# Kernel optimization log

Measured on AMD Instinct MI355X. Metric: run time of the kernel, lower is better.

The kernel has to match this reference:

```python
import jax, jax.numpy as jnp
import numpy as np

BN_EPS = 1e-5

def _vq(x, embed):
    # x: (..., dim), embed: (dim, K). Nearest-codeword lookup with straight-through.
    dim = x.shape[-1]
    flat = x.reshape(-1, dim)
    dist = (flat * flat).sum(1, keepdims=True) - 2.0 * (flat @ embed) + (embed * embed).sum(0, keepdims=True)
    ids = jnp.argmin(dist, axis=1)
    q = jnp.take(embed.T, ids, axis=0).reshape(x.shape)
    diff = jnp.mean((jax.lax.stop_gradient(q) - x) ** 2)
    q = x + jax.lax.stop_gradient(q - x)
    return q, diff

def _weight_quantize(W, embed, in_mem, out_mem):
    # W: (out_f, in_f). Group W.T into (out_g, in_g, in_mem*out_mem) blocks,
    # VQ each block, scatter back to (out_f, in_f). Matches torch chunk/stack loops.
    out_f, in_f = W.shape
    in_g, out_g = in_f // in_mem, out_f // out_mem
    g = W.T.reshape(in_g, in_mem, out_g, out_mem).transpose(2, 0, 1, 3).reshape(out_g, in_g, in_mem * out_mem)
    q, diff = _vq(g, embed)
    qW = q.reshape(out_g, in_g, in_mem, out_mem).transpose(0, 3, 1, 2).reshape(out_f, in_f)
    return qW, diff

def _bn(x, gamma, beta):
    # training-mode BatchNorm1d: biased batch variance
    mu = x.mean(axis=0)
    var = ((x - mu) ** 2).mean(axis=0)
    return (x - mu) * jax.lax.rsqrt(var + BN_EPS) * gamma + beta


def setup_inputs() -> dict:
    key = jax.random.key(0)
    ks = jax.random.split(key, 8)
    B, D_IN, H, D_OUT, K = 65536, 784, 512, 10, 512
    s = 0.05
    return {
        "x": jax.random.normal(ks[0], (B, D_IN), jnp.float32),
        "W1": jax.random.normal(ks[1], (H, D_IN), jnp.float32) * s,
        "b1": jnp.zeros((H,), jnp.float32),
        "gamma1": jnp.ones((H,), jnp.float32),
        "beta1": jnp.zeros((H,), jnp.float32),
        "E1": jax.random.normal(ks[2], (28, K), jnp.float32) * s,  # dim = in_mem(7)*out_mem(4)
        "W2": jax.random.normal(ks[3], (H, H), jnp.float32) * s,
        "b2": jnp.zeros((H,), jnp.float32),
        "E2": jax.random.normal(ks[4], (16, K), jnp.float32) * s,  # dim = in_mem(16)*out_mem(1)
        "W3": jax.random.normal(ks[5], (D_OUT, H), jnp.float32) * s,
        "b3": jnp.zeros((D_OUT,), jnp.float32),
    }


def reference(x, W1, b1, gamma1, beta1, E1, W2, b2, E2, W3, b3):
    qW1, diff1 = _weight_quantize(W1, E1, 7, 4)
    h = jax.nn.relu(x @ qW1.T + b1)
    qW2, diff2 = _weight_quantize(W2, E2, 16, 1)
    h = jax.nn.relu(_bn(h, gamma1, beta1) @ qW2.T + b2)
    out = h @ W3.T + b3
    return out, diff1 + diff2
```

## Files before the change

### kernel.cpp

```cpp
#include <hip/hip_runtime.h>
#include <stdint.h>

#define BATCH   65536
#define D_IN    784
#define KP      800
#define HDIM    512
#define D_OUT   10
#define NCODE   512
#define HT_LD   520

typedef _Float16 f16;
typedef _Float16 f16x8 __attribute__((ext_vector_type(8)));
typedef float    f32x4 __attribute__((ext_vector_type(4)));

__device__ __forceinline__ void gld_lds16(const void* g, void* l) {
  __builtin_amdgcn_global_load_lds((const __attribute__((address_space(1))) void*)g,
                                   (__attribute__((address_space(3))) void*)l, 16, 0, 0);
}

#define MEMFENCE asm volatile("" ::: "memory")
#define BARRIER() do { MEMFENCE; __builtin_amdgcn_s_barrier(); MEMFENCE; } while (0)

__global__ void k_vq1(const float* __restrict__ W1, const float* __restrict__ E1,
                      f16* __restrict__ qW1, float* __restrict__ diffacc) {
  #pragma clang fp contract(off)
  __shared__ float E1s[28 * NCODE];
  __shared__ float Ts[NCODE];
  for (int i = threadIdx.x; i < 28 * NCODE; i += 256) E1s[i] = E1[i];
  __syncthreads();
  for (int k = threadIdx.x; k < NCODE; k += 256) {
    float e0 = E1s[k];
    float t = e0 * e0;
    for (int j = 1; j < 28; ++j) {
      float e = E1s[j * NCODE + k];
      float ee = e * e;
      t = t + ee;
    }
    Ts[k] = t;
  }
  __syncthreads();
  const int wid = threadIdx.x >> 6, lane = threadIdx.x & 63;
  const int bid = blockIdx.x * 4 + wid;
  const int og = bid / 112, ig = bid % 112;
  float v[28], vv[28];
  #pragma unroll
  for (int j = 0; j < 28; ++j) {
    int om = j & 3, im = j >> 2;
    v[j] = W1[(og * 4 + om) * D_IN + ig * 7 + im];
    vv[j] = v[j] * v[j];
  }
  float r[8];
  #pragma unroll
  for (int j = 0; j < 8; ++j) r[j] = vv[j];
  #pragma unroll
  for (int j = 0; j < 8; ++j) r[j] = r[j] + vv[8 + j];
  #pragma unroll
  for (int j = 0; j < 8; ++j) r[j] = r[j] + vv[16 + j];
  float s = ((r[0] + r[1]) + (r[2] + r[3])) + ((r[4] + r[5]) + (r[6] + r[7]));
  s = s + vv[24]; s = s + vv[25]; s = s + vv[26]; s = s + vv[27];

  float bestd = 1e30f; int bestk = 0x7fffffff;
  for (int t = 0; t < 8; ++t) {
    int k = t * 64 + lane;
    float dot = 0.f;
    #pragma unroll
    for (int j = 0; j < 28; ++j) dot = __builtin_fmaf(v[j], E1s[j * NCODE + k], dot);
    float d = (s - 2.0f * dot) + Ts[k];
    if (d < bestd || (d == bestd && k < bestk)) { bestd = d; bestk = k; }
  }
  for (int off = 32; off; off >>= 1) {
    float d2 = __shfl_down(bestd, off, 64);
    int   k2 = __shfl_down(bestk, off, 64);
    if (d2 < bestd || (d2 == bestd && k2 < bestk)) { bestd = d2; bestk = k2; }
  }
  int kstar = __shfl(bestk, 0, 64);
  float sq = 0.f;
  if (lane < 28) {
    int om = lane & 3, im = lane >> 2;
    float q = E1s[lane * NCODE + kstar];
    qW1[(size_t)(og * 4 + om) * KP + ig * 7 + im] = (f16)q;
    float dd = q - v[lane]; sq = dd * dd;
  }
  for (int off = 32; off; off >>= 1) sq += __shfl_down(sq, off, 64);
  if (lane == 0) atomicAdd(&diffacc[bid & 127], sq);
}

__global__ void k_vq2(const float* __restrict__ W2, const float* __restrict__ E2,
                      f16* __restrict__ qW2, float* __restrict__ diffacc) {
  #pragma clang fp contract(off)
  __shared__ float E2s[16 * NCODE];
  __shared__ float Ts[NCODE];
  for (int i = threadIdx.x; i < 16 * NCODE; i += 256) E2s[i] = E2[i];
  __syncthreads();
  for (int k = threadIdx.x; k < NCODE; k += 256) {
    float e0 = E2s[k];
    float t = e0 * e0;
    for (int j = 1; j < 16; ++j) {
      float e = E2s[j * NCODE + k];
      float ee = e * e;
      t = t + ee;
    }
    Ts[k] = t;
  }
  __syncthreads();
  const int wid = threadIdx.x >> 6, lane = threadIdx.x & 63;
  const int bid = blockIdx.x * 4 + wid;
  const int og = bid >> 5, ig = bid & 31;
  float v[16], vv[16];
  #pragma unroll
  for (int j = 0; j < 16; ++j) {
    v[j] = W2[og * HDIM + ig * 16 + j];
    vv[j] = v[j] * v[j];
  }
  float r[8];
  #pragma unroll
  for (int j = 0; j < 8; ++j) r[j] = vv[j];
  #pragma unroll
  for (int j = 0; j < 8; ++j) r[j] = r[j] + vv[8 + j];
  float s = ((r[0] + r[1]) + (r[2] + r[3])) + ((r[4] + r[5]) + (r[6] + r[7]));

  float bestd = 1e30f; int bestk = 0x7fffffff;
  for (int t = 0; t < 8; ++t) {
    int k = t * 64 + lane;
    float dot = 0.f;
    #pragma unroll
    for (int j = 0; j < 16; ++j) dot = __builtin_fmaf(v[j], E2s[j * NCODE + k], dot);
    float d = (s - 2.0f * dot) + Ts[k];
    if (d < bestd || (d == bestd && k < bestk)) { bestd = d; bestk = k; }
  }
  for (int off = 32; off; off >>= 1) {
    float d2 = __shfl_down(bestd, off, 64);
    int   k2 = __shfl_down(bestk, off, 64);
    if (d2 < bestd || (d2 == bestd && k2 < bestk)) { bestd = d2; bestk = k2; }
  }
  int kstar = __shfl(bestk, 0, 64);
  float sq = 0.f;
  if (lane < 16) {
    float q = E2s[lane * NCODE + kstar];
    qW2[(size_t)og * HDIM + ig * 16 + lane] = (f16)q;
    float dd = q - v[lane]; sq = dd * dd;
  }
  for (int off = 32; off; off >>= 1) sq += __shfl_down(sq, off, 64);
  if (lane == 0) atomicAdd(&diffacc[bid & 127], sq);
}

__global__ void __launch_bounds__(512, 2)
k_gemm1(const float* __restrict__ X, const f16* __restrict__ Bw,
        const float* __restrict__ bias, f16* __restrict__ C,
        float* __restrict__ statacc) {
  __shared__ __align__(16) char lds_all[HT_LD * 128 * 2];
  __shared__ float cls[512], cls2[512];
  f16* ht = (f16*)lds_all;
  const int tid = threadIdx.x;
  const int bm = blockIdx.x;
  const int lane = tid & 63, wid = tid >> 6;
  const int waveM = wid & 1, waveN = wid >> 1;
  const int l15 = lane & 15, quad = lane >> 4;

  cls[tid] = 0.f; cls2[tid] = 0.f;

  const int rA = tid >> 2, cA = tid & 3;
  const float* gArow = X + (size_t)(bm * 128 + rA) * D_IN;
  const int wAoff = rA * 32 + ((cA ^ ((rA >> 1) & 3)) * 8);
  const f16* gBp[4]; int lBoff[4];
  #pragma unroll
  for (int i = 0; i < 4; ++i) {
    int s = tid + i * 512;
    int rB = s >> 2, cB = s & 3;
    gBp[i] = Bw + (size_t)rB * KP + ((cB ^ ((rB >> 1) & 3)) * 8);
    lBoff[i] = s * 8;
  }

  f32x4 acc[4][8];
  #pragma unroll
  for (int i = 0; i < 4; ++i)
    #pragma unroll
    for (int j = 0; j < 8; ++j) acc[i][j] = (f32x4){0.f, 0.f, 0.f, 0.f};

  const int cs_l = (l15 >> 1) & 3;
  const int aoff = (waveM * 64 + l15) * 32;
  const int boff = (waveN * 128 + l15) * 32;
  const int qoff = (quad ^ cs_l) * 8;

  float4 ra0, ra1;
  auto issueA = [&](int k0) {
    int gc = k0 + cA * 8;
    int gco = gc < D_IN ? gc : 0;
    ra0 = *(const float4*)(gArow + gco);
    ra1 = *(const float4*)(gArow + gco + 4);
  };
  auto writeA = [&](int k0, char* buf) {
    float4 a0 = ra0, a1 = ra1;
    if (k0 + cA * 8 >= D_IN) { a0 = (float4){0.f,0.f,0.f,0.f}; a1 = a0; }
    f16x8 o;
    o[0]=(f16)a0.x; o[1]=(f16)a0.y; o[2]=(f16)a0.z; o[3]=(f16)a0.w;
    o[4]=(f16)a1.x; o[5]=(f16)a1.y; o[6]=(f16)a1.z; o[7]=(f16)a1.w;
    *(f16x8*)((f16*)buf + wAoff) = o;
  };
  auto issueB = [&](int k0, char* buf) {
    f16* Bs_ = (f16*)(buf + 8192);
    #pragma unroll
    for (int i = 0; i < 4; ++i) gld_lds16(gBp[i] + k0, Bs_ + lBoff[i]);
  };
  auto mma = [&](const char* buf) {
    const f16* As_ = (const f16*)buf;
    const f16* Bs_ = (const f16*)(buf + 8192);
    f16x8 af[4], bf[8];
    #pragma unroll
    for (int i = 0; i < 4; ++i) af[i] = *(const f16x8*)(As_ + aoff + i * 512 + qoff);
    #pragma unroll
    for (int j = 0; j < 8; ++j) bf[j] = *(const f16x8*)(Bs_ + boff + j * 512 + qoff);
    #pragma unroll
    for (int i = 0; i < 4; ++i)
      #pragma unroll
      for (int j = 0; j < 8; ++j)
        acc[i][j] = __builtin_amdgcn_mfma_f32_16x16x32_f16(af[i], bf[j], acc[i][j], 0, 0, 0);
  };

  const int NT = KP / 32;

  issueA(0);  MEMFENCE;
  issueB(0, lds_all);          MEMFENCE;
  issueB(32, lds_all + 40960); MEMFENCE;
  writeA(0, lds_all);
  MEMFENCE;
  issueA(32); MEMFENCE;
  asm volatile("s_waitcnt vmcnt(6) lgkmcnt(0)" ::: "memory");
  BARRIER();

  int cur = 0;
  for (int k = 0; k < NT; ++k) {
    int n1 = cur + 40960; if (n1 == 122880) n1 = 0;
    int n2 = n1 + 40960;  if (n2 == 122880) n2 = 0;
    if (k + 2 < NT) { issueB((k + 2) * 32, lds_all + n2); }
    MEMFENCE;
    __builtin_amdgcn_s_setprio(1);
    mma(lds_all + cur);
    __builtin_amdgcn_s_setprio(0);
    if (k + 1 < NT) {
      MEMFENCE;
      writeA((k + 1) * 32, lds_all + n1);
      MEMFENCE;
      if (k + 2 < NT) {
        issueA((k + 2) * 32); MEMFENCE;
        asm volatile("s_waitcnt vmcnt(6) lgkmcnt(0)" ::: "memory");
      } else {
        asm volatile("s_waitcnt vmcnt(0) lgkmcnt(0)" ::: "memory");
      }
    }
    BARRIER();
    cur = n1;
  }

  const int colbase = waveN * 128 + l15;
  float bcol[8];
  #pragma unroll
  for (int j = 0; j < 8; ++j) bcol[j] = bias[colbase + j * 16];
  float cs[8], cs2[8];
  #pragma unroll
  for (int j = 0; j < 8; ++j) { cs[j] = 0.f; cs2[j] = 0.f; }
  #pragma unroll
  for (int i = 0; i < 4; ++i)
    #pragma unroll
    for (int r2 = 0; r2 < 4; ++r2) {
      int rloc = waveM * 64 + i * 16 + quad * 4 + r2;
      #pragma unroll
      for (int j = 0; j < 8; ++j) {
        float v = acc[i][j][r2] + bcol[j];
        v = v > 0.f ? v : 0.f;
        ht[rloc * HT_LD + waveN * 128 + j * 16 + l15] = (f16)v;
        cs[j] += v; cs2[j] += v * v;
      }
    }
  #pragma unroll
  for (int j = 0; j < 8; ++j) {
    cs[j]  += __shfl_xor(cs[j], 16, 64);  cs[j]  += __shfl_xor(cs[j], 32, 64);
    cs2[j] += __shfl_xor(cs2[j], 16, 64); cs2[j] += __shfl_xor(cs2[j], 32, 64);
  }
  if (quad == 0) {
    #pragma unroll
    for (int j = 0; j < 8; ++j) {
      atomicAdd(&cls[waveN * 128 + j * 16 + l15], cs[j]);
      atomicAdd(&cls2[waveN * 128 + j * 16 + l15], cs2[j]);
    }
  }
  __syncthreads();
  atomicAdd(&statacc[256 + tid], cls[tid]);
  atomicAdd(&statacc[768 + tid], cls2[tid]);
  #pragma unroll
  for (int rr = 0; rr < 16; ++rr) {
    int row = wid * 16 + rr;
    f16x8 vrow = *(const f16x8*)(ht + row * HT_LD + lane * 8);
    *(f16x8*)(C + (size_t)(bm * 128 + row) * HDIM + lane * 8) = vrow;
  }
}

__global__ void k_bnprep(const float* __restrict__ acc, const float* __restrict__ gamma,
                         const float* __restrict__ beta, float* __restrict__ ab,
                         const float* __restrict__ W3, f16* __restrict__ W3h,
                         float* __restrict__ diff_out) {
  const int c = threadIdx.x;
  const float inv = 1.f / 65536.f;
  float mu = acc[256 + c] * inv;
  float msq = acc[768 + c] * inv;
  float var = msq - mu * mu;
  float a = gamma[c] / sqrtf(var + 1e-5f);
  ab[c] = a;
  ab[512 + c] = beta[c] - mu * a;
  #pragma unroll
  for (int o = 0; o < 16; ++o)
    W3h[o * HDIM + c] = (o < D_OUT) ? (f16)W3[o * HDIM + c] : (f16)0.f;
  if (c == 0) {
    float s1 = 0.f, s2 = 0.f;
    for (int i = 0; i < 128; ++i) { s1 += acc[i]; s2 += acc[128 + i]; }
    diff_out[0] = s1 * (1.f / 401408.f) + s2 * (1.f / 262144.f);
  }
}

__global__ void k_bnfold(f16* __restrict__ qW2, const float* __restrict__ ab,
                         const float* __restrict__ b2, float* __restrict__ bias2) {
  __shared__ float red[256];
  const int n = blockIdx.x, t = threadIdx.x;
  float partial = 0.f;
  #pragma unroll
  for (int kk = 0; kk < 2; ++kk) {
    int k = t + kk * 256;
    float w = (float)qW2[n * HDIM + k];
    partial += ab[512 + k] * w;
    qW2[n * HDIM + k] = (f16)(ab[k] * w);
  }
  red[t] = partial; __syncthreads();
  for (int s = 128; s > 0; s >>= 1) { if (t < s) red[t] += red[t + s]; __syncthreads(); }
  if (t == 0) bias2[n] = b2[n] + red[0];
}

__global__ void __launch_bounds__(512, 2)
k_gemm2f(const f16* __restrict__ A, const f16* __restrict__ Bw,
         const float* __restrict__ bias2, const f16* __restrict__ W3h,
         const float* __restrict__ b3, float* __restrict__ out) {
  __shared__ __align__(16) char lds_all[HT_LD * 128 * 2];
  f16* ht = (f16*)lds_all;
  const int tid = threadIdx.x;
  const int bm = blockIdx.x;
  const int lane = tid & 63, wid = tid >> 6;
  const int waveM = wid & 1, waveN = wid >> 1;
  const int l15 = lane & 15, quad = lane >> 4;

  const int rA = tid >> 2, cA = tid & 3;
  const f16* gAp = A + (size_t)(bm * 128 + rA) * HDIM + ((cA ^ ((rA >> 1) & 3)) * 8);
  const int lAoff = tid * 8;
  const f16* gBp[4]; int lBoff[4];
  #pragma unroll
  for (int i = 0; i < 4; ++i) {
    int s = tid + i * 512;
    int rB = s >> 2, cB = s & 3;
    gBp[i] = Bw + (size_t)rB * HDIM + ((cB ^ ((rB >> 1) & 3)) * 8);
    lBoff[i] = s * 8;
  }

  f32x4 acc[4][8];
  #pragma unroll
  for (int i = 0; i < 4; ++i)
    #pragma unroll
    for (int j = 0; j < 8; ++j) acc[i][j] = (f32x4){0.f, 0.f, 0.f, 0.f};

  const int cs_l = (l15 >> 1) & 3;
  const int aoff = (waveM * 64 + l15) * 32;
  const int boff = (waveN * 128 + l15) * 32;
  const int qoff = (quad ^ cs_l) * 8;

  auto issueT = [&](int k0, char* buf) {
    f16* As_ = (f16*)buf;
    f16* Bs_ = (f16*)(buf + 8192);
    gld_lds16(gAp + k0, As_ + lAoff);
    #pragma unroll
    for (int i = 0; i < 4; ++i) gld_lds16(gBp[i] + k0, Bs_ + lBoff[i]);
  };
  auto mma = [&](const char* buf) {
    const f16* As_ = (const f16*)buf;
    const f16* Bs_ = (const f16*)(buf + 8192);
    f16x8 af[4], bf[8];
    #pragma unroll
    for (int i = 0; i < 4; ++i) af[i] = *(const f16x8*)(As_ + aoff + i * 512 + qoff);
    #pragma unroll
    for (int j = 0; j < 8; ++j) bf[j] = *(const f16x8*)(Bs_ + boff + j * 512 + qoff);
    #pragma unroll
    for (int i = 0; i < 4; ++i)
      #pragma unroll
      for (int j = 0; j < 8; ++j)
        acc[i][j] = __builtin_amdgcn_mfma_f32_16x16x32_f16(af[i], bf[j], acc[i][j], 0, 0, 0);
  };

  const int NT = HDIM / 32;

  issueT(0, lds_all);          MEMFENCE;
  issueT(32, lds_all + 40960); MEMFENCE;
  asm volatile("s_waitcnt vmcnt(5)" ::: "memory");
  BARRIER();

  int cur = 0;
  for (int k = 0; k < NT; ++k) {
    int n1 = cur + 40960; if (n1 == 122880) n1 = 0;
    int n2 = n1 + 40960;  if (n2 == 122880) n2 = 0;
    if (k + 2 < NT) { issueT((k + 2) * 32, lds_all + n2); }
    MEMFENCE;
    __builtin_amdgcn_s_setprio(1);
    mma(lds_all + cur);
    __builtin_amdgcn_s_setprio(0);
    if (k + 2 < NT)      asm volatile("s_waitcnt vmcnt(5)" ::: "memory");
    else if (k + 1 < NT) asm volatile("s_waitcnt vmcnt(0)" ::: "memory");
    BARRIER();
    cur = n1;
  }

  const int colbase = waveN * 128 + l15;
  float bcol[8];
  #pragma unroll
  for (int j = 0; j < 8; ++j) bcol[j] = bias2[colbase + j * 16];
  #pragma unroll
  for (int i = 0; i < 4; ++i)
    #pragma unroll
    for (int r2 = 0; r2 < 4; ++r2) {
      int rloc = waveM * 64 + i * 16 + quad * 4 + r2;
      #pragma unroll
      for (int j = 0; j < 8; ++j) {
        float v = acc[i][j][r2] + bcol[j];
        v = v > 0.f ? v : 0.f;
        ht[rloc * HT_LD + waveN * 128 + j * 16 + l15] = (f16)v;
      }
    }
  __syncthreads();
  f32x4 oacc = (f32x4){0.f, 0.f, 0.f, 0.f};
  #pragma unroll
  for (int ks = 0; ks < 16; ++ks) {
    f16x8 bfr = *(const f16x8*)(W3h + l15 * HDIM + ks * 32 + quad * 8);
    f16x8 afr = *(const f16x8*)(ht + (wid * 16 + l15) * HT_LD + ks * 32 + quad * 8);
    oacc = __builtin_amdgcn_mfma_f32_16x16x32_f16(afr, bfr, oacc, 0, 0, 0);
  }
  if (l15 < D_OUT) {
    float badd = b3[l15];
    #pragma unroll
    for (int r2 = 0; r2 < 4; ++r2) {
      int row = bm * 128 + wid * 16 + quad * 4 + r2;
      out[(size_t)row * D_OUT + l15] = oacc[r2] + badd;
    }
  }
}

extern "C" void kernel_launch(void* const* d_in, const int* in_sizes, int n_in,
                              void* d_out, int out_size, void* d_ws, size_t ws_size,
                              hipStream_t stream) {
  const float* x     = (const float*)d_in[0];
  const float* W1    = (const float*)d_in[1];
  const float* b1    = (const float*)d_in[2];
  const float* gamma = (const float*)d_in[3];
  const float* beta  = (const float*)d_in[4];
  const float* E1    = (const float*)d_in[5];
  const float* W2    = (const float*)d_in[6];
  const float* b2    = (const float*)d_in[7];
  const float* E2    = (const float*)d_in[8];
  const float* W3    = (const float*)d_in[9];
  const float* b3    = (const float*)d_in[10];
  float* out = (float*)d_out;

  char* ws = (char*)d_ws;
  float* accum = (float*)ws;
  f16* qW1h = (f16*)(ws + 8192);
  f16* qW2h = (f16*)(ws + 827392);
  f16* W3h  = (f16*)(ws + 1351680);
  float* ab = (float*)(ws + 1368064);
  float* bias2 = (float*)(ws + 1372160);
  f16* h    = (f16*)(ws + 1376256);

  (void)hipMemsetAsync(ws, 0, 827392, stream);
  k_vq1<<<3584, 256, 0, stream>>>(W1, E1, qW1h, accum);
  k_vq2<<<4096, 256, 0, stream>>>(W2, E2, qW2h, accum + 128);
  k_gemm1<<<512, 512, 0, stream>>>(x, qW1h, b1, h, accum);
  k_bnprep<<<1, 512, 0, stream>>>(accum, gamma, beta, ab, W3, W3h, out + (size_t)BATCH * D_OUT);
  k_bnfold<<<512, 256, 0, stream>>>(qW2h, ab, b2, bias2);
  k_gemm2f<<<512, 512, 0, stream>>>(h, qW2h, bias2, W3h, b3, out);
}
```

Baseline: 516.6 us.

## Switch GEMM mainloops to BK=64 with single A buffer and double-buffered B

```diff
diff --git a/kernel.cpp b/kernel.cpp
--- a/kernel.cpp
+++ b/kernel.cpp
@@ -3,7 +3,7 @@
 
 #define BATCH   65536
 #define D_IN    784
-#define KP      800
+#define KP      832
 #define HDIM    512
 #define D_OUT   10
 #define NCODE   512
@@ -148,7 +148,7 @@
 k_gemm1(const float* __restrict__ X, const f16* __restrict__ Bw,
         const float* __restrict__ bias, f16* __restrict__ C,
         float* __restrict__ statacc) {
-  __shared__ __align__(16) char lds_all[HT_LD * 128 * 2];
+  __shared__ __align__(16) char lds_all[147456];
   __shared__ float cls[512], cls2[512];
   f16* ht = (f16*)lds_all;
   const int tid = threadIdx.x;
@@ -161,13 +161,14 @@
 
   const int rA = tid >> 2, cA = tid & 3;
   const float* gArow = X + (size_t)(bm * 128 + rA) * D_IN;
-  const int wAoff = rA * 32 + ((cA ^ ((rA >> 1) & 3)) * 8);
-  const f16* gBp[4]; int lBoff[4];
-  #pragma unroll
-  for (int i = 0; i < 4; ++i) {
+  const int wA0 = rA * 64 + ((cA ^ (rA & 7)) * 8);
+  const int wA1 = rA * 64 + (((cA + 4) ^ (rA & 7)) * 8);
+  const f16* gBp[8]; int lBoff[8];
+  #pragma unroll
+  for (int i = 0; i < 8; ++i) {
     int s = tid + i * 512;
-    int rB = s >> 2, cB = s & 3;
-    gBp[i] = Bw + (size_t)rB * KP + ((cB ^ ((rB >> 1) & 3)) * 8);
+    int rB = s >> 3, cB = s & 7;
+    gBp[i] = Bw + (size_t)rB * KP + ((cB ^ (rB & 7)) * 8);
     lBoff[i] = s * 8;
   }
 
@@ -177,80 +178,78 @@
     #pragma unroll
     for (int j = 0; j < 8; ++j) acc[i][j] = (f32x4){0.f, 0.f, 0.f, 0.f};
 
-  const int cs_l = (l15 >> 1) & 3;
-  const int aoff = (waveM * 64 + l15) * 32;
-  const int boff = (waveN * 128 + l15) * 32;
-  const int qoff = (quad ^ cs_l) * 8;
-
-  float4 ra0, ra1;
+  const int swz = (l15 & 7);
+  const int arow = waveM * 64 + l15;
+  const int brow = waveN * 128 + l15;
+
+  float4 ra0, ra1, ra2, ra3;
   auto issueA = [&](int k0) {
-    int gc = k0 + cA * 8;
-    int gco = gc < D_IN ? gc : 0;
-    ra0 = *(const float4*)(gArow + gco);
-    ra1 = *(const float4*)(gArow + gco + 4);
-  };
-  auto writeA = [&](int k0, char* buf) {
-    float4 a0 = ra0, a1 = ra1;
-    if (k0 + cA * 8 >= D_IN) { a0 = (float4){0.f,0.f,0.f,0.f}; a1 = a0; }
-    f16x8 o;
-    o[0]=(f16)a0.x; o[1]=(f16)a0.y; o[2]=(f16)a0.z; o[3]=(f16)a0.w;
-    o[4]=(f16)a1.x; o[5]=(f16)a1.y; o[6]=(f16)a1.z; o[7]=(f16)a1.w;
-    *(f16x8*)((f16*)buf + wAoff) = o;
-  };
-  auto issueB = [&](int k0, char* buf) {
-    f16* Bs_ = (f16*)(buf + 8192);
-    #pragma unroll
-    for (int i = 0; i < 4; ++i) gld_lds16(gBp[i] + k0, Bs_ + lBoff[i]);
-  };
-  auto mma = [&](const char* buf) {
-    const f16* As_ = (const f16*)buf;
-    const f16* Bs_ = (const f16*)(buf + 8192);
-    f16x8 af[4], bf[8];
-    #pragma unroll
-    for (int i = 0; i < 4; ++i) af[i] = *(const f16x8*)(As_ + aoff + i * 512 + qoff);
-    #pragma unroll
-    for (int j = 0; j < 8; ++j) bf[j] = *(const f16x8*)(Bs_ + boff + j * 512 + qoff);
-    #pragma unroll
-    for (int i = 0; i < 4; ++i)
-      #pragma unroll
-      for (int j = 0; j < 8; ++j)
-        acc[i][j] = __builtin_amdgcn_mfma_f32_16x16x32_f16(af[i], bf[j], acc[i][j], 0, 0, 0);
-  };
-
-  const int NT = KP / 32;
-
+    int g0 = k0 + cA * 8;
+    int g1 = k0 + (cA + 4) * 8;
+    int g0c = g0 < D_IN ? g0 : 0;
+    int g1c = g1 < D_IN ? g1 : 0;
+    ra0 = *(const float4*)(gArow + g0c);
+    ra1 = *(const float4*)(gArow + g0c + 4);
+    ra2 = *(const float4*)(gArow + g1c);
+    ra3 = *(const float4*)(gArow + g1c + 4);
+  };
+  auto writeA = [&](int k0) {
+    float4 a0 = ra0, a1 = ra1, b0 = ra2, b1 = ra3;
+    if (k0 + cA * 8 >= D_IN)       { a0 = (float4){0.f,0.f,0.f,0.f}; a1 = a0; }
+    if (k0 + (cA + 4) * 8 >= D_IN) { b0 = (float4){0.f,0.f,0.f,0.f}; b1 = b0; }
+    f16x8 o0, o1;
+    o0[0]=(f16)a0.x; o0[1]=(f16)a0.y; o0[2]=(f16)a0.z; o0[3]=(f16)a0.w;
+    o0[4]=(f16)a1.x; o0[5]=(f16)a1.y; o0[6]=(f16)a1.z; o0[7]=(f16)a1.w;
+    o1[0]=(f16)b0.x; o1[1]=(f16)b0.y; o1[2]=(f16)b0.z; o1[3]=(f16)b0.w;
+    o1[4]=(f16)b1.x; o1[5]=(f16)b1.y; o1[6]=(f16)b1.z; o1[7]=(f16)b1.w;
+    *(f16x8*)((f16*)lds_all + wA0) = o0;
+    *(f16x8*)((f16*)lds_all + wA1) = o1;
+  };
+  auto issueB = [&](int k0, int bOff) {
+    f16* Bs_ = (f16*)(lds_all + bOff);
+    #pragma unroll
+    for (int i = 0; i < 8; ++i) gld_lds16(gBp[i] + k0, Bs_ + lBoff[i]);
+  };
+  auto mma = [&](int bOff) {
+    const f16* As_ = (const f16*)lds_all;
+    const f16* Bs_ = (const f16*)(lds_all + bOff);
+    #pragma unroll
+    for (int ks = 0; ks < 2; ++ks) {
+      const int coff = ((ks * 4 + quad) ^ swz) * 8;
+      f16x8 af[4], bf[8];
+      #pragma unroll
+      for (int i = 0; i < 4; ++i) af[i] = *(const f16x8*)(As_ + (arow + i * 16) * 64 + coff);
+      #pragma unroll
+      for (int j = 0; j < 8; ++j) bf[j] = *(const f16x8*)(Bs_ + (brow + j * 16) * 64 + coff);
+      #pragma unroll
+      for (int i = 0; i < 4; ++i)
+        #pragma unroll
+        for (int j = 0; j < 8; ++j)
+          acc[i][j] = __builtin_amdgcn_mfma_f32_16x16x32_f16(af[i], bf[j], acc[i][j], 0, 0, 0);
+    }
+  };
+
+  const int NT = KP / 64;
   issueA(0);  MEMFENCE;
-  issueB(0, lds_all);          MEMFENCE;
-  issueB(32, lds_all + 40960); MEMFENCE;
-  writeA(0, lds_all);
-  MEMFENCE;
-  issueA(32); MEMFENCE;
-  asm volatile("s_waitcnt vmcnt(6) lgkmcnt(0)" ::: "memory");
-  BARRIER();
-
-  int cur = 0;
+  issueB(0, 16384); MEMFENCE;
+
   for (int k = 0; k < NT; ++k) {
-    int n1 = cur + 40960; if (n1 == 122880) n1 = 0;
-    int n2 = n1 + 40960;  if (n2 == 122880) n2 = 0;
-    if (k + 2 < NT) { issueB((k + 2) * 32, lds_all + n2); }
+    BARRIER();
+    writeA(k * 64);
     MEMFENCE;
+    if (k + 1 < NT) {
+      issueA((k + 1) * 64); MEMFENCE;
+      issueB((k + 1) * 64, 16384 + ((k + 1) & 1) * 65536); MEMFENCE;
+      asm volatile("s_waitcnt vmcnt(12) lgkmcnt(0)" ::: "memory");
+    } else {
+      asm volatile("s_waitcnt vmcnt(0) lgkmcnt(0)" ::: "memory");
+    }
+    BARRIER();
     __builtin_amdgcn_s_setprio(1);
-    mma(lds_all + cur);
+    mma(16384 + (k & 1) * 65536);
     __builtin_amdgcn_s_setprio(0);
-    if (k + 1 < NT) {
-      MEMFENCE;
-      writeA((k + 1) * 32, lds_all + n1);
-      MEMFENCE;
-      if (k + 2 < NT) {
-        issueA((k + 2) * 32); MEMFENCE;
-        asm volatile("s_waitcnt vmcnt(6) lgkmcnt(0)" ::: "memory");
-      } else {
-        asm volatile("s_waitcnt vmcnt(0) lgkmcnt(0)" ::: "memory");
-      }
-    }
-    BARRIER();
-    cur = n1;
-  }
+  }
+  __syncthreads();
 
   const int colbase = waveN * 128 + l15;
   float bcol[8];
@@ -338,7 +337,7 @@
 k_gemm2f(const f16* __restrict__ A, const f16* __restrict__ Bw,
          const float* __restrict__ bias2, const f16* __restrict__ W3h,
          const float* __restrict__ b3, float* __restrict__ out) {
-  __shared__ __align__(16) char lds_all[HT_LD * 128 * 2];
+  __shared__ __align__(16) char lds_all[147456];
   f16* ht = (f16*)lds_all;
   const int tid = threadIdx.x;
   const int bm = blockIdx.x;
@@ -347,14 +346,15 @@
   const int l15 = lane & 15, quad = lane >> 4;
 
   const int rA = tid >> 2, cA = tid & 3;
-  const f16* gAp = A + (size_t)(bm * 128 + rA) * HDIM + ((cA ^ ((rA >> 1) & 3)) * 8);
-  const int lAoff = tid * 8;
-  const f16* gBp[4]; int lBoff[4];
-  #pragma unroll
-  for (int i = 0; i < 4; ++i) {
+  const f16* gArow = A + (size_t)(bm * 128 + rA) * HDIM;
+  const int wA0 = rA * 64 + ((cA ^ (rA & 7)) * 8);
+  const int wA1 = rA * 64 + (((cA + 4) ^ (rA & 7)) * 8);
+  const f16* gBp[8]; int lBoff[8];
+  #pragma unroll
+  for (int i = 0; i < 8; ++i) {
     int s = tid + i * 512;
-    int rB = s >> 2, cB = s & 3;
-    gBp[i] = Bw + (size_t)rB * HDIM + ((cB ^ ((rB >> 1) & 3)) * 8);
+    int rB = s >> 3, cB = s & 7;
+    gBp[i] = Bw + (size_t)rB * HDIM + ((cB ^ (rB & 7)) * 8);
     lBoff[i] = s * 8;
   }
 
@@ -364,54 +364,64 @@
     #pragma unroll
     for (int j = 0; j < 8; ++j) acc[i][j] = (f32x4){0.f, 0.f, 0.f, 0.f};
 
-  const int cs_l = (l15 >> 1) & 3;
-  const int aoff = (waveM * 64 + l15) * 32;
-  const int boff = (waveN * 128 + l15) * 32;
-  const int qoff = (quad ^ cs_l) * 8;
-
-  auto issueT = [&](int k0, char* buf) {
-    f16* As_ = (f16*)buf;
-    f16* Bs_ = (f16*)(buf + 8192);
-    gld_lds16(gAp + k0, As_ + lAoff);
-    #pragma unroll
-    for (int i = 0; i < 4; ++i) gld_lds16(gBp[i] + k0, Bs_ + lBoff[i]);
-  };
-  auto mma = [&](const char* buf) {
-    const f16* As_ = (const f16*)buf;
-    const f16* Bs_ = (const f16*)(buf + 8192);
-    f16x8 af[4], bf[8];
-    #pragma unroll
-    for (int i = 0; i < 4; ++i) af[i] = *(const f16x8*)(As_ + aoff + i * 512 + qoff);
-    #pragma unroll
-    for (int j = 0; j < 8; ++j) bf[j] = *(const f16x8*)(Bs_ + boff + j * 512 + qoff);
-    #pragma unroll
-    for (int i = 0; i < 4; ++i)
-      #pragma unroll
-      for (int j = 0; j < 8; ++j)
-        acc[i][j] = __builtin_amdgcn_mfma_f32_16x16x32_f16(af[i], bf[j], acc[i][j], 0, 0, 0);
-  };
-
-  const int NT = HDIM / 32;
-
-  issueT(0, lds_all);          MEMFENCE;
-  issueT(32, lds_all + 40960); MEMFENCE;
-  asm volatile("s_waitcnt vmcnt(5)" ::: "memory");
-  BARRIER();
-
-  int cur = 0;
+  const int swz = (l15 & 7);
+  const int arow = waveM * 64 + l15;
+  const int brow = waveN * 128 + l15;
+
+  f16x8 ra0, ra1;
+  auto issueA = [&](int k0) {
+    ra0 = *(const f16x8*)(gArow + k0 + cA * 8);
+    ra1 = *(const f16x8*)(gArow + k0 + (cA + 4) * 8);
+  };
+  auto writeA = [&]() {
+    *(f16x8*)((f16*)lds_all + wA0) = ra0;
+    *(f16x8*)((f16*)lds_all + wA1) = ra1;
+  };
+  auto issueB = [&](int k0, int bOff) {
+    f16* Bs_ = (f16*)(lds_all + bOff);
+    #pragma unroll
+    for (int i = 0; i < 8; ++i) gld_lds16(gBp[i] + k0, Bs_ + lBoff[i]);
+  };
+  auto mma = [&](int bOff) {
+    const f16* As_ = (const f16*)lds_all;
+    const f16* Bs_ = (const f16*)(lds_all + bOff);
+    #pragma unroll
+    for (int ks = 0; ks < 2; ++ks) {
+      const int coff = ((ks * 4 + quad) ^ swz) * 8;
+      f16x8 af[4], bf[8];
+      #pragma unroll
+      for (int i = 0; i < 4; ++i) af[i] = *(const f16x8*)(As_ + (arow + i * 16) * 64 + coff);
+      #pragma unroll
+      for (int j = 0; j < 8; ++j) bf[j] = *(const f16x8*)(Bs_ + (brow + j * 16) * 64 + coff);
+      #pragma unroll
+      for (int i = 0; i < 4; ++i)
+        #pragma unroll
+        for (int j = 0; j < 8; ++j)
+          acc[i][j] = __builtin_amdgcn_mfma_f32_16x16x32_f16(af[i], bf[j], acc[i][j], 0, 0, 0);
+    }
+  };
+
+  const int NT = HDIM / 64;
+  issueA(0);  MEMFENCE;
+  issueB(0, 16384); MEMFENCE;
+
   for (int k = 0; k < NT; ++k) {
-    int n1 = cur + 40960; if (n1 == 122880) n1 = 0;
-    int n2 = n1 + 40960;  if (n2 == 122880) n2 = 0;
-    if (k + 2 < NT) { issueT((k + 2) * 32, lds_all + n2); }
+    BARRIER();
+    writeA();
     MEMFENCE;
+    if (k + 1 < NT) {
+      issueA((k + 1) * 64); MEMFENCE;
+      issueB((k + 1) * 64, 16384 + ((k + 1) & 1) * 65536); MEMFENCE;
+      asm volatile("s_waitcnt vmcnt(10) lgkmcnt(0)" ::: "memory");
+    } else {
+      asm volatile("s_waitcnt vmcnt(0) lgkmcnt(0)" ::: "memory");
+    }
+    BARRIER();
     __builtin_amdgcn_s_setprio(1);
-    mma(lds_all + cur);
+    mma(16384 + (k & 1) * 65536);
     __builtin_amdgcn_s_setprio(0);
-    if (k + 2 < NT)      asm volatile("s_waitcnt vmcnt(5)" ::: "memory");
-    else if (k + 1 < NT) asm volatile("s_waitcnt vmcnt(0)" ::: "memory");
-    BARRIER();
-    cur = n1;
-  }
+  }
+  __syncthreads();
 
   const int colbase = waveN * 128 + l15;
   float bcol[8];
@@ -466,13 +476,13 @@
   char* ws = (char*)d_ws;
   float* accum = (float*)ws;
   f16* qW1h = (f16*)(ws + 8192);
-  f16* qW2h = (f16*)(ws + 827392);
-  f16* W3h  = (f16*)(ws + 1351680);
-  float* ab = (float*)(ws + 1368064);
-  float* bias2 = (float*)(ws + 1372160);
-  f16* h    = (f16*)(ws + 1376256);
-
-  (void)hipMemsetAsync(ws, 0, 827392, stream);
+  f16* qW2h = (f16*)(ws + 860160);
+  f16* W3h  = (f16*)(ws + 1384448);
+  float* ab = (float*)(ws + 1400832);
+  float* bias2 = (float*)(ws + 1404928);
+  f16* h    = (f16*)(ws + 1409024);
+
+  (void)hipMemsetAsync(ws, 0, 860160, stream);
   k_vq1<<<3584, 256, 0, stream>>>(W1, E1, qW1h, accum);
   k_vq2<<<4096, 256, 0, stream>>>(W2, E2, qW2h, accum + 128);
   k_gemm1<<<512, 512, 0, stream>>>(x, qW1h, b1, h, accum);
```

New measurement: 515.1 us. About the same (-0.3%).
